# Kernel optimization log

Measured on AMD Instinct MI355X. Metric: run time of the kernel, lower is better.

## Reference

```python
import jax, jax.numpy as jnp
import numpy as np

SEQ, BATCH, EMBED = 1024, 2, 768
E = 16            # num_experts = m * N = 2 * 8
FFN_H = 1536      # expert_dim = ceil(3072 / 2)
K_SHARED = 1
K_ROUTE = 3       # (m * top_k) - k_shared = 4 - 1
LN_EPS = 1e-5
NEG_INF = -1e9


def setup_inputs() -> dict:
    key = jax.random.key(0)
    ks = jax.random.split(key, 4)
    x = jax.random.normal(ks[0], (SEQ, BATCH, EMBED), dtype=jnp.float32)
    gate_w = jax.random.normal(ks[1], (EMBED, E), dtype=jnp.float32) * 0.02
    gate_b = jnp.zeros((E,), jnp.float32)
    fc1_w = jax.random.normal(ks[2], (E, EMBED, FFN_H), dtype=jnp.float32) * 0.02
    fc1_b = jnp.zeros((E, FFN_H), jnp.float32)
    ln_w = jnp.ones((E, FFN_H), jnp.float32)
    ln_b = jnp.zeros((E, FFN_H), jnp.float32)
    fc2_w = jax.random.normal(ks[3], (E, FFN_H, EMBED), dtype=jnp.float32) * 0.02
    fc2_b = jnp.zeros((E, EMBED), jnp.float32)
    return {"x": x, "gate_w": gate_w, "gate_b": gate_b,
            "fc1_w": fc1_w, "fc1_b": fc1_b, "ln_w": ln_w, "ln_b": ln_b,
            "fc2_w": fc2_w, "fc2_b": fc2_b}


def reference(x, gate_w, gate_b, fc1_w, fc1_b, ln_w, ln_b, fc2_w, fc2_b):
    S, B, D = x.shape
    T = S * B
    xf = x.reshape(T, D)

    # --- gating: mask shared-expert logits, softmax, top-k over routed probs ---
    scores = xf @ gate_w + gate_b                      # [T, E]
    scores = scores.at[:, :K_SHARED].set(NEG_INF)
    probs = jax.nn.softmax(scores, axis=-1)
    topv, topi = jax.lax.top_k(probs, K_ROUTE)         # [T, K_ROUTE]

    # combine weights: gate prob for selected routed experts, 1.0 for shared experts
    combine = jnp.zeros((T, E), xf.dtype)
    combine = combine.at[jnp.arange(T)[:, None], topi].add(topv)
    combine = combine.at[:, :K_SHARED].add(1.0)        # shared expert(s), weight 1

    # --- per-expert FFN (dense over experts; combine zeros out unselected) ---
    h = jnp.einsum('td,edh->eth', xf, fc1_w) + fc1_b[:, None, :]   # [E, T, H]
    h = jax.nn.gelu(h, approximate=False)              # torch nn.GELU = exact erf
    mu = h.mean(-1, keepdims=True)
    var = h.var(-1, keepdims=True)
    h = (h - mu) * jax.lax.rsqrt(var + LN_EPS) * ln_w[:, None, :] + ln_b[:, None, :]
    y = jnp.einsum('eth,ehd->etd', h, fc2_w) + fc2_b[:, None, :]   # [E, T, D]

    # --- scatter-add combine (gate-weighted sum over experts) ---
    out = jnp.einsum('te,etd->td', combine, y)
    return out.reshape(S, B, D)
```

## Files before the change

kernel.cpp:

```cpp
#include <hip/hip_runtime.h>
#include <cmath>

#define T_TOK 2048
#define D_EMB 768
#define H_FFN 1536
#define NE    16
#define NPAIR (T_TOK * 4)

#define NT1   4608
#define NT2   4608
#define NCONV 2048
#define NGATE 512

typedef __attribute__((ext_vector_type(8))) short          short8;
typedef __attribute__((ext_vector_type(8))) unsigned short ushort8;
typedef __attribute__((ext_vector_type(4))) unsigned short ushort4v;
typedef __attribute__((ext_vector_type(4))) float          floatx4;

__device__ __forceinline__ float bf2f(unsigned short u) {
  union { unsigned int i; float f; } v; v.i = ((unsigned int)u) << 16; return v.f;
}
__device__ __forceinline__ unsigned short f2bf(float f) {
  union { float f; unsigned int i; } v; v.f = f;
  unsigned int r = v.i + 0x7fffu + ((v.i >> 16) & 1u);
  return (unsigned short)(r >> 16);
}

__device__ __forceinline__ void gload16(const unsigned short* g, unsigned short* l) {
  __builtin_amdgcn_global_load_lds(
      (const __attribute__((address_space(1))) unsigned int*)g,
      (__attribute__((address_space(3))) unsigned int*)l,
      16, 0, 0);
}

__device__ __forceinline__ int block_sniff(const unsigned int* __restrict__ xw, int tid) {
  int c = 0;
#pragma unroll
  for (int i = 0; i < 2; i++) {
    unsigned int w = xw[tid * 2 + i];
    unsigned int e = (w >> 7) & 0xFFu;
    c += (e >= 100u && e <= 140u) ? 1 : 0;
  }
#pragma unroll
  for (int off = 32; off > 0; off >>= 1) c += __shfl_down(c, off);
  __shared__ int ssn[4];
  int wave = tid >> 6, lane = tid & 63;
  if (lane == 0) ssn[wave] = c;
  __syncthreads();
  return (ssn[0] + ssn[1] + ssn[2] + ssn[3] > 300) ? 1 : 0;
}

template<int R, int C>
__device__ __forceinline__ void transpose_body(
    const unsigned short* __restrict__ srcB, const float* __restrict__ srcF,
    int isbf, unsigned short* __restrict__ dst, int bx, int tid,
    unsigned char* smemraw)
{
  auto tile = (unsigned short(*)[72])smemraw;
  constexpr int RT = R / 64, CT = C / 64;
  int e   = bx / (RT * CT);
  int rem = bx % (RT * CT);
  int rt  = rem / CT, ct = rem % CT;
  int r   = tid >> 2;
  int c   = (tid & 3) * 16;
  int xr  = (r & 7) * 8;
  size_t sbase = ((size_t)e * R + rt * 64 + r) * C + ct * 64 + c;
  if (isbf) {
    ushort8 v0 = *(const ushort8*)(srcB + sbase);
    ushort8 v1 = *(const ushort8*)(srcB + sbase + 8);
    *(ushort8*)&tile[r][(c) ^ xr]     = v0;
    *(ushort8*)&tile[r][(c + 8) ^ xr] = v1;
  } else {
    unsigned short tmp[16];
#pragma unroll
    for (int q = 0; q < 4; q++) {
      floatx4 f = *(const floatx4*)(srcF + sbase + q * 4);
#pragma unroll
      for (int j = 0; j < 4; j++) tmp[q * 4 + j] = f2bf(f[j]);
    }
    *(ushort8*)&tile[r][(c) ^ xr]     = *(ushort8*)&tmp[0];
    *(ushort8*)&tile[r][(c + 8) ^ xr] = *(ushort8*)&tmp[8];
  }
  __syncthreads();
  int n  = tid >> 2;
  int k  = (tid & 3) * 16;
  unsigned short outv[16];
#pragma unroll
  for (int j = 0; j < 16; j++) {
    int kr = k + j;
    outv[j] = tile[kr][n ^ ((kr & 7) * 8)];
  }
  size_t dbase = ((size_t)e * C + ct * 64 + n) * R + rt * 64 + k;
  *(ushort8*)(dst + dbase)     = *(ushort8*)&outv[0];
  *(ushort8*)(dst + dbase + 8) = *(ushort8*)&outv[8];
}

__global__ __launch_bounds__(256) void prep_kernel(
    const unsigned int* __restrict__ xw,
    const unsigned short* __restrict__ x16, const float* __restrict__ x32,
    const unsigned short* __restrict__ gw16, const float* __restrict__ gw32,
    const unsigned short* __restrict__ gb16, const float* __restrict__ gb32,
    const unsigned short* __restrict__ w1B, const float* __restrict__ w1F,
    const unsigned short* __restrict__ w2B, const float* __restrict__ w2F,
    const float* __restrict__ fc1bF, const float* __restrict__ lnwF,
    const float* __restrict__ lnbF, const float* __restrict__ fc2bF,
    unsigned short* __restrict__ xC,
    unsigned short* __restrict__ dfc1b, unsigned short* __restrict__ dlnw,
    unsigned short* __restrict__ dlnb, unsigned short* __restrict__ dfc2b,
    unsigned short* __restrict__ fc1T, unsigned short* __restrict__ fc2T,
    int* __restrict__ flagOut,
    int* __restrict__ psel, float* __restrict__ pw,
    int* __restrict__ cnt, int* __restrict__ plist)
{
  __shared__ __align__(16) unsigned char smem[4 * 64 * 17 * 4];
  int bid = blockIdx.x;
  int tid = threadIdx.x;
  int isbf = block_sniff(xw, tid);
  if (bid == 0 && tid == 0) *flagOut = isbf;

  if (bid < NT1) {
    transpose_body<768, 1536>(w1B, w1F, isbf, fc1T, bid, tid, smem);
  } else if (bid < NT1 + NT2) {
    transpose_body<1536, 768>(w2B, w2F, isbf, fc2T, bid - NT1, tid, smem);
  } else if (bid < NT1 + NT2 + NCONV) {
    if (!isbf) {
      int g = (bid - NT1 - NT2) * 256 + tid;
#pragma unroll
      for (int i = 0; i < 3; i++) xC[g + i * 524288] = f2bf(x32[g + i * 524288]);
      if (g < 24576) { dfc1b[g] = f2bf(fc1bF[g]); dlnw[g] = f2bf(lnwF[g]); dlnb[g] = f2bf(lnbF[g]); }
      if (g < 12288) dfc2b[g] = f2bf(fc2bF[g]);
    }
  } else {
    int wave = tid >> 6, lane = tid & 63;
    int t = (bid - (NT1 + NT2 + NCONV)) * 4 + wave;
    float acc[NE];
#pragma unroll
    for (int e = 0; e < NE; e++) acc[e] = 0.f;
    if (isbf) {
#pragma unroll
      for (int i = 0; i < D_EMB / 64; i++) {
        int d = i * 64 + lane;
        float xv = bf2f(x16[(size_t)t * D_EMB + d]);
        ushort8 g0 = *(const ushort8*)(gw16 + d * NE);
        ushort8 g1 = *(const ushort8*)(gw16 + d * NE + 8);
#pragma unroll
        for (int e = 0; e < 8; e++) acc[e]     += xv * bf2f(g0[e]);
#pragma unroll
        for (int e = 0; e < 8; e++) acc[8 + e] += xv * bf2f(g1[e]);
      }
    } else {
#pragma unroll
      for (int i = 0; i < D_EMB / 64; i++) {
        int d = i * 64 + lane;
        float xv = x32[(size_t)t * D_EMB + d];
#pragma unroll
        for (int q = 0; q < 4; q++) {
          floatx4 g = *(const floatx4*)(gw32 + d * NE + q * 4);
#pragma unroll
          for (int j = 0; j < 4; j++) acc[q * 4 + j] += xv * g[j];
        }
      }
    }
    auto sacc = (float(*)[64][17])smem;
#pragma unroll
    for (int e = 0; e < NE; e++) sacc[wave][lane][e] = acc[e];
    __syncthreads();
    int e = lane & 15, q = lane >> 4;
    float s = 0.f;
#pragma unroll
    for (int i = 0; i < 16; i++) s += sacc[wave][q * 16 + i][e];
    s += __shfl_xor(s, 16);
    s += __shfl_xor(s, 32);
    float sv = s + (isbf ? bf2f(gb16[e]) : gb32[e]);
    if (e == 0) sv = -1e9f;
    float m = sv;
#pragma unroll
    for (int off = 8; off > 0; off >>= 1) m = fmaxf(m, __shfl_xor(m, off));
    float pe = expf(sv - m);
    float den = pe;
#pragma unroll
    for (int off = 8; off > 0; off >>= 1) den += __shfl_xor(den, off);
    float pr = pe / den;
    float val = (e == 0) ? -1.f : pr;
    int sel0, sel1, sel2; float sw0, sw1, sw2;
#pragma unroll
    for (int k = 0; k < 3; k++) {
      float bv = val; int bi = e;
#pragma unroll
      for (int off = 8; off > 0; off >>= 1) {
        float ov = __shfl_xor(bv, off);
        int   oi = __shfl_xor(bi, off);
        if (ov > bv || (ov == bv && oi < bi)) { bv = ov; bi = oi; }
      }
      if (k == 0) { sel0 = bi; sw0 = bv; }
      else if (k == 1) { sel1 = bi; sw1 = bv; }
      else { sel2 = bi; sw2 = bv; }
      if (e == bi) val = -1.f;
    }
    if (lane < 4) {
      int se; float swt;
      if (lane == 0)      { se = 0;    swt = 1.0f; }
      else if (lane == 1) { se = sel0; swt = sw0; }
      else if (lane == 2) { se = sel1; swt = sw1; }
      else                { se = sel2; swt = sw2; }
      int pidx = t * 4 + lane;
      psel[pidx] = se; pw[pidx] = swt;
      int pos = atomicAdd(&cnt[se], 1);
      plist[se * T_TOK + pos] = pidx;
    }
  }
}

template<int KDIM, int NDIM, bool GELU, bool HASBIAS, bool AROWDIV4, bool OUTF32>
__global__ __launch_bounds__(256) void moe_gemm(
    const unsigned short* __restrict__ AO, const unsigned short* __restrict__ AC,
    const unsigned short* __restrict__ BT,
    const unsigned short* __restrict__ biasO, const unsigned short* __restrict__ biasC,
    const int* __restrict__ flag,
    const int* __restrict__ cnt, const int* __restrict__ plist,
    unsigned short* __restrict__ outB, float* __restrict__ outF)
{
  const int NSP = NDIM / 128;
  int bx  = blockIdx.x;
  int e   = bx / (16 * NSP);
  int rem = bx % (16 * NSP);
  int mt  = rem / NSP;
  int ns  = rem % NSP;
  int count = cnt[e];
  if (mt * 128 >= count) return;
  const unsigned short* Abase   = (*flag) ? AO : AC;
  const unsigned short* biasAll = (*flag) ? biasO : biasC;

  __shared__ __align__(16) unsigned short sA[128 * 64];
  __shared__ __align__(16) unsigned short sB[128 * 64];
  __shared__ int sp[128];

  int tid = threadIdx.x;
  if (tid < 128) {
    int rg  = mt * 128 + tid;
    int idx = rg < count ? rg : count - 1;
    sp[tid] = plist[e * T_TOK + idx];
  }
  __syncthreads();

  int lane = tid & 63;
  int wave = tid >> 6;
  int n0   = ns * 128;

  int lrow  = lane >> 3;
  int lsch  = (lane & 7) ^ lrow;
  const unsigned short* ag[4];
  const unsigned short* bg[4];
  int loff[4];
#pragma unroll
  for (int s = 0; s < 4; s++) {
    int r  = wave * 32 + s * 8;
    int p  = sp[r + lrow];
    ag[s] = Abase + (size_t)(AROWDIV4 ? (p >> 2) : p) * KDIM + lsch * 8;
    bg[s] = BT + ((size_t)e * NDIM + n0 + r + lrow) * KDIM + lsch * 8;
    loff[s] = r * 64;
  }

  int m16  = lane & 15;
  int quad = lane >> 4;
  int wm   = (wave >> 1) * 64;
  int wn   = (wave & 1) * 64;
  int rsw  = (m16 & 7);

  floatx4 acc[4][4];
#pragma unroll
  for (int i = 0; i < 4; i++)
#pragma unroll
    for (int j = 0; j < 4; j++) acc[i][j] = (floatx4){0.f, 0.f, 0.f, 0.f};

  for (int k0 = 0; k0 < KDIM; k0 += 64) {
    if (k0) __syncthreads();
#pragma unroll
    for (int s = 0; s < 4; s++) gload16(ag[s] + k0, sA + loff[s]);
#pragma unroll
    for (int s = 0; s < 4; s++) gload16(bg[s] + k0, sB + loff[s]);
    __syncthreads();
#pragma unroll
    for (int ks = 0; ks < 2; ks++) {
      int ch = ((ks * 4 + quad) ^ rsw) * 8;
      short8 af[4], bf[4];
#pragma unroll
      for (int m = 0; m < 4; m++)
        af[m] = *(const short8*)(sA + (wm + m * 16 + m16) * 64 + ch);
#pragma unroll
      for (int n = 0; n < 4; n++)
        bf[n] = *(const short8*)(sB + (wn + n * 16 + m16) * 64 + ch);
#pragma unroll
      for (int m = 0; m < 4; m++)
#pragma unroll
        for (int n = 0; n < 4; n++)
          acc[m][n] = __builtin_amdgcn_mfma_f32_16x16x32_bf16(af[m], bf[n], acc[m][n], 0, 0, 0);
    }
  }

#pragma unroll
  for (int m = 0; m < 4; m++) {
#pragma unroll
    for (int r = 0; r < 4; r++) {
      int row_local = wm + m * 16 + quad * 4 + r;
      int rg = mt * 128 + row_local;
      if (rg < count) {
        int p = sp[row_local];
#pragma unroll
        for (int n = 0; n < 4; n++) {
          int col = n0 + wn + n * 16 + m16;
          float v = acc[m][n][r];
          if (HASBIAS) v += bf2f(biasAll[e * NDIM + col]);
          if (GELU)    v = 0.5f * v * (1.f + erff(v * 0.70710678118654752f));
          if (OUTF32) outF[(size_t)p * NDIM + col] = v;
          else        outB[(size_t)p * NDIM + col] = f2bf(v);
        }
      }
    }
  }
}

__global__ __launch_bounds__(256) void ln_kernel(
    unsigned short* __restrict__ Hbuf,
    const unsigned short* __restrict__ lnwO, const unsigned short* __restrict__ lnwC,
    const unsigned short* __restrict__ lnbO, const unsigned short* __restrict__ lnbC,
    const int* __restrict__ psel, const float* __restrict__ pw,
    const int* __restrict__ flag)
{
  int p = blockIdx.x;
  int tid = threadIdx.x;
  int e = psel[p];
  int isbf = *flag;
  const unsigned short* lnw = isbf ? lnwO : lnwC;
  const unsigned short* lnb = isbf ? lnbO : lnbC;
  unsigned short* hr = Hbuf + (size_t)p * H_FFN;
  bool act = tid < 192;
  float v[8];
  float s = 0.f, sq = 0.f;
  if (act) {
    ushort8 hv = *(const ushort8*)(hr + tid * 8);
#pragma unroll
    for (int j = 0; j < 8; j++) { v[j] = bf2f(hv[j]); s += v[j]; sq += v[j] * v[j]; }
  }
#pragma unroll
  for (int off = 32; off > 0; off >>= 1) {
    s  += __shfl_down(s, off);
    sq += __shfl_down(sq, off);
  }
  __shared__ float red[8];
  int wave = tid >> 6, lane = tid & 63;
  if (lane == 0) { red[wave * 2] = s; red[wave * 2 + 1] = sq; }
  __syncthreads();
  __shared__ float mv[2];
  if (tid == 0) {
    float S = 0.f, Q = 0.f;
    for (int w = 0; w < 4; w++) { S += red[w * 2]; Q += red[w * 2 + 1]; }
    float mu  = S * (1.f / H_FFN);
    float var = Q * (1.f / H_FFN) - mu * mu;
    mv[0] = mu; mv[1] = rsqrtf(var + 1e-5f);
  }
  __syncthreads();
  if (act) {
    float mu = mv[0], rstd = mv[1];
    float w = pw[p];
    ushort8 lw = *(const ushort8*)(lnw + e * H_FFN + tid * 8);
    ushort8 lb = *(const ushort8*)(lnb + e * H_FFN + tid * 8);
    ushort8 o;
#pragma unroll
    for (int j = 0; j < 8; j++)
      o[j] = f2bf(((v[j] - mu) * rstd * bf2f(lw[j]) + bf2f(lb[j])) * w);
    *(ushort8*)(hr + tid * 8) = o;
  }
}

__global__ __launch_bounds__(192) void combine_kernel(
    const float* __restrict__ Y,
    const unsigned short* __restrict__ b2O, const unsigned short* __restrict__ b2C,
    const int* __restrict__ psel, const float* __restrict__ pw,
    unsigned short* __restrict__ out16, float* __restrict__ out32,
    const int* __restrict__ flag)
{
  int t = blockIdx.x;
  int tid = threadIdx.x;
  int isbf = *flag;
  const unsigned short* b2 = isbf ? b2O : b2C;
  int e1 = psel[t * 4 + 1], e2 = psel[t * 4 + 2], e3 = psel[t * 4 + 3];
  float w1 = pw[t * 4 + 1], w2 = pw[t * 4 + 2], w3 = pw[t * 4 + 3];
  int d = tid * 4;
  const float* Yb = Y + (size_t)t * 4 * D_EMB + d;
  floatx4 y0 = *(const floatx4*)(Yb);
  floatx4 y1 = *(const floatx4*)(Yb + D_EMB);
  floatx4 y2 = *(const floatx4*)(Yb + 2 * D_EMB);
  floatx4 y3 = *(const floatx4*)(Yb + 3 * D_EMB);
  ushort4v b0 = *(const ushort4v*)(b2 + d);
  ushort4v bb1 = *(const ushort4v*)(b2 + e1 * D_EMB + d);
  ushort4v bb2 = *(const ushort4v*)(b2 + e2 * D_EMB + d);
  ushort4v bb3 = *(const ushort4v*)(b2 + e3 * D_EMB + d);
  if (isbf) {
    ushort4v o;
#pragma unroll
    for (int j = 0; j < 4; j++) {
      float a = y0[j] + y1[j] + y2[j] + y3[j] + bf2f(b0[j])
              + w1 * bf2f(bb1[j]) + w2 * bf2f(bb2[j]) + w3 * bf2f(bb3[j]);
      o[j] = f2bf(a);
    }
    *(ushort4v*)(out16 + (size_t)t * D_EMB + d) = o;
  } else {
    floatx4 o;
#pragma unroll
    for (int j = 0; j < 4; j++)
      o[j] = y0[j] + y1[j] + y2[j] + y3[j] + bf2f(b0[j])
           + w1 * bf2f(bb1[j]) + w2 * bf2f(bb2[j]) + w3 * bf2f(bb3[j]);
    *(floatx4*)(out32 + (size_t)t * D_EMB + d) = o;
  }
}

extern "C" void kernel_launch(void* const* d_in, const int* in_sizes, int n_in,
                              void* d_out, int out_size, void* d_ws, size_t ws_size,
                              hipStream_t stream)
{
  (void)in_sizes; (void)n_in; (void)out_size; (void)ws_size;
  char* ws = (char*)d_ws;
  int*   cnt   = (int*)ws;
  int*   plist = (int*)(ws + 256);
  int*   psel  = (int*)(ws + 131328);
  float* pw    = (float*)(ws + 164096);
  int*   flag  = (int*)(ws + 196864);
  unsigned short* fc1bC = (unsigned short*)(ws + 197120);
  unsigned short* lnwC  = (unsigned short*)(ws + 246272);
  unsigned short* lnbC  = (unsigned short*)(ws + 295424);
  unsigned short* fc2bC = (unsigned short*)(ws + 344576);
  unsigned short* xC    = (unsigned short*)(ws + 524288);
  unsigned short* Hbuf  = (unsigned short*)(ws + 3670016);
  float*          Ybuf  = (float*)(ws + 28835840);
  unsigned short* fc1T  = (unsigned short*)(ws + 54001664);
  unsigned short* fc2T  = (unsigned short*)(ws + 91750400);

  hipMemsetAsync(cnt, 0, 64, stream);

  prep_kernel<<<NT1 + NT2 + NCONV + NGATE, 256, 0, stream>>>(
      (const unsigned int*)d_in[0],
      (const unsigned short*)d_in[0], (const float*)d_in[0],
      (const unsigned short*)d_in[1], (const float*)d_in[1],
      (const unsigned short*)d_in[2], (const float*)d_in[2],
      (const unsigned short*)d_in[3], (const float*)d_in[3],
      (const unsigned short*)d_in[7], (const float*)d_in[7],
      (const float*)d_in[4], (const float*)d_in[5],
      (const float*)d_in[6], (const float*)d_in[8],
      xC, fc1bC, lnwC, lnbC, fc2bC,
      fc1T, fc2T,
      flag, psel, pw, cnt, plist);

  moe_gemm<D_EMB, H_FFN, true, true, true, false>
      <<<NE * 16 * (H_FFN / 128), 256, 0, stream>>>(
      (const unsigned short*)d_in[0], xC, fc1T,
      (const unsigned short*)d_in[4], fc1bC,
      flag, cnt, plist, Hbuf, nullptr);

  ln_kernel<<<NPAIR, 256, 0, stream>>>(
      Hbuf,
      (const unsigned short*)d_in[5], lnwC,
      (const unsigned short*)d_in[6], lnbC,
      psel, pw, flag);

  moe_gemm<H_FFN, D_EMB, false, false, false, true>
      <<<NE * 16 * (D_EMB / 128), 256, 0, stream>>>(
      Hbuf, Hbuf, fc2T,
      nullptr, nullptr,
      flag, cnt, plist, nullptr, Ybuf);

  combine_kernel<<<T_TOK, 192, 0, stream>>>(
      Ybuf,
      (const unsigned short*)d_in[8], fc2bC,
      psel, pw,
      (unsigned short*)d_out, (float*)d_out, flag);
}
```

Baseline: 354.2 us.

## Drop weight transpose pass; read K-major weights via LDS transpose loads

The prep kernel no longer transposes fc1/fc2 weights into N-major layout. It now does a plain vectorised fp32->bf16 conversion, or nothing when inputs are already bf16. The GEMM loads B tiles in their original K×N layout into LDS and uses ds_read_b64_tr_b16 to build the MFMA B fragments, removing the transpose's LDS round trip and strided writes. The cost is an explicit lgkmcnt wait and sched barrier in the inner loop, plus an LDS tile layout that may bank-conflict.

```diff
diff --git a/kernel.cpp b/kernel.cpp
--- a/kernel.cpp
+++ b/kernel.cpp
@@ -7,12 +7,14 @@
 #define NE    16
 #define NPAIR (T_TOK * 4)
 
-#define NT1   4608
-#define NT2   4608
-#define NCONV 2048
+#define NW1   9216
+#define NW2   9216
+#define NX    768
+#define NB    12
 #define NGATE 512
 
 typedef __attribute__((ext_vector_type(8))) short          short8;
+typedef __attribute__((ext_vector_type(4))) short          short4v;
 typedef __attribute__((ext_vector_type(8))) unsigned short ushort8;
 typedef __attribute__((ext_vector_type(4))) unsigned short ushort4v;
 typedef __attribute__((ext_vector_type(4))) float          floatx4;
@@ -31,6 +33,17 @@
       (const __attribute__((address_space(1))) unsigned int*)g,
       (__attribute__((address_space(3))) unsigned int*)l,
       16, 0, 0);
+}
+
+__device__ __forceinline__ unsigned ldsaddr(const void* p) {
+  return (unsigned)(unsigned long long)
+      (const __attribute__((address_space(3))) char*)p;
+}
+
+__device__ __forceinline__ short4v tr8(unsigned a) {
+  short4v d;
+  asm volatile("ds_read_b64_tr_b16 %0, %1" : "=v"(d) : "v"(a));
+  return d;
 }
 
 __device__ __forceinline__ int block_sniff(const unsigned int* __restrict__ xw, int tid) {
@@ -50,49 +63,14 @@
   return (ssn[0] + ssn[1] + ssn[2] + ssn[3] > 300) ? 1 : 0;
 }
 
-template<int R, int C>
-__device__ __forceinline__ void transpose_body(
-    const unsigned short* __restrict__ srcB, const float* __restrict__ srcF,
-    int isbf, unsigned short* __restrict__ dst, int bx, int tid,
-    unsigned char* smemraw)
-{
-  auto tile = (unsigned short(*)[72])smemraw;
-  constexpr int RT = R / 64, CT = C / 64;
-  int e   = bx / (RT * CT);
-  int rem = bx % (RT * CT);
-  int rt  = rem / CT, ct = rem % CT;
-  int r   = tid >> 2;
-  int c   = (tid & 3) * 16;
-  int xr  = (r & 7) * 8;
-  size_t sbase = ((size_t)e * R + rt * 64 + r) * C + ct * 64 + c;
-  if (isbf) {
-    ushort8 v0 = *(const ushort8*)(srcB + sbase);
-    ushort8 v1 = *(const ushort8*)(srcB + sbase + 8);
-    *(ushort8*)&tile[r][(c) ^ xr]     = v0;
-    *(ushort8*)&tile[r][(c + 8) ^ xr] = v1;
-  } else {
-    unsigned short tmp[16];
-#pragma unroll
-    for (int q = 0; q < 4; q++) {
-      floatx4 f = *(const floatx4*)(srcF + sbase + q * 4);
-#pragma unroll
-      for (int j = 0; j < 4; j++) tmp[q * 4 + j] = f2bf(f[j]);
-    }
-    *(ushort8*)&tile[r][(c) ^ xr]     = *(ushort8*)&tmp[0];
-    *(ushort8*)&tile[r][(c + 8) ^ xr] = *(ushort8*)&tmp[8];
-  }
-  __syncthreads();
-  int n  = tid >> 2;
-  int k  = (tid & 3) * 16;
-  unsigned short outv[16];
-#pragma unroll
-  for (int j = 0; j < 16; j++) {
-    int kr = k + j;
-    outv[j] = tile[kr][n ^ ((kr & 7) * 8)];
-  }
-  size_t dbase = ((size_t)e * C + ct * 64 + n) * R + rt * 64 + k;
-  *(ushort8*)(dst + dbase)     = *(ushort8*)&outv[0];
-  *(ushort8*)(dst + dbase + 8) = *(ushort8*)&outv[8];
+__device__ __forceinline__ void conv8(const float* __restrict__ src,
+                                      unsigned short* __restrict__ dst, size_t i) {
+  floatx4 a = *(const floatx4*)(src + i);
+  floatx4 b = *(const floatx4*)(src + i + 4);
+  ushort8 o;
+#pragma unroll
+  for (int j = 0; j < 4; j++) { o[j] = f2bf(a[j]); o[4 + j] = f2bf(b[j]); }
+  *(ushort8*)(dst + i) = o;
 }
 
 __global__ __launch_bounds__(256) void prep_kernel(
@@ -100,39 +78,41 @@
     const unsigned short* __restrict__ x16, const float* __restrict__ x32,
     const unsigned short* __restrict__ gw16, const float* __restrict__ gw32,
     const unsigned short* __restrict__ gb16, const float* __restrict__ gb32,
-    const unsigned short* __restrict__ w1B, const float* __restrict__ w1F,
-    const unsigned short* __restrict__ w2B, const float* __restrict__ w2F,
+    const float* __restrict__ w1F, const float* __restrict__ w2F,
     const float* __restrict__ fc1bF, const float* __restrict__ lnwF,
     const float* __restrict__ lnbF, const float* __restrict__ fc2bF,
     unsigned short* __restrict__ xC,
+    unsigned short* __restrict__ wsW1, unsigned short* __restrict__ wsW2,
     unsigned short* __restrict__ dfc1b, unsigned short* __restrict__ dlnw,
     unsigned short* __restrict__ dlnb, unsigned short* __restrict__ dfc2b,
-    unsigned short* __restrict__ fc1T, unsigned short* __restrict__ fc2T,
     int* __restrict__ flagOut,
     int* __restrict__ psel, float* __restrict__ pw,
     int* __restrict__ cnt, int* __restrict__ plist)
 {
-  __shared__ __align__(16) unsigned char smem[4 * 64 * 17 * 4];
+  __shared__ __align__(16) float sacc[4][64][17];
   int bid = blockIdx.x;
   int tid = threadIdx.x;
   int isbf = block_sniff(xw, tid);
   if (bid == 0 && tid == 0) *flagOut = isbf;
 
-  if (bid < NT1) {
-    transpose_body<768, 1536>(w1B, w1F, isbf, fc1T, bid, tid, smem);
-  } else if (bid < NT1 + NT2) {
-    transpose_body<1536, 768>(w2B, w2F, isbf, fc2T, bid - NT1, tid, smem);
-  } else if (bid < NT1 + NT2 + NCONV) {
+  if (bid < NW1) {
+    if (!isbf) conv8(w1F, wsW1, ((size_t)bid * 256 + tid) * 8);
+  } else if (bid < NW1 + NW2) {
+    if (!isbf) conv8(w2F, wsW2, ((size_t)(bid - NW1) * 256 + tid) * 8);
+  } else if (bid < NW1 + NW2 + NX) {
+    if (!isbf) conv8(x32, xC, ((size_t)(bid - NW1 - NW2) * 256 + tid) * 8);
+  } else if (bid < NW1 + NW2 + NX + NB) {
     if (!isbf) {
-      int g = (bid - NT1 - NT2) * 256 + tid;
-#pragma unroll
-      for (int i = 0; i < 3; i++) xC[g + i * 524288] = f2bf(x32[g + i * 524288]);
-      if (g < 24576) { dfc1b[g] = f2bf(fc1bF[g]); dlnw[g] = f2bf(lnwF[g]); dlnb[g] = f2bf(lnbF[g]); }
-      if (g < 12288) dfc2b[g] = f2bf(fc2bF[g]);
+      size_t g = (size_t)(bid - NW1 - NW2 - NX) * 256 + tid;
+      size_t i = g * 8;
+      conv8(fc1bF, dfc1b, i);
+      conv8(lnwF,  dlnw,  i);
+      conv8(lnbF,  dlnb,  i);
+      if (g < 1536) conv8(fc2bF, dfc2b, i);
     }
   } else {
     int wave = tid >> 6, lane = tid & 63;
-    int t = (bid - (NT1 + NT2 + NCONV)) * 4 + wave;
+    int t = (bid - (NW1 + NW2 + NX + NB)) * 4 + wave;
     float acc[NE];
 #pragma unroll
     for (int e = 0; e < NE; e++) acc[e] = 0.f;
@@ -161,7 +141,6 @@
         }
       }
     }
-    auto sacc = (float(*)[64][17])smem;
 #pragma unroll
     for (int e = 0; e < NE; e++) sacc[wave][lane][e] = acc[e];
     __syncthreads();
@@ -214,7 +193,7 @@
 template<int KDIM, int NDIM, bool GELU, bool HASBIAS, bool AROWDIV4, bool OUTF32>
 __global__ __launch_bounds__(256) void moe_gemm(
     const unsigned short* __restrict__ AO, const unsigned short* __restrict__ AC,
-    const unsigned short* __restrict__ BT,
+    const unsigned short* __restrict__ BO, const unsigned short* __restrict__ BC,
     const unsigned short* __restrict__ biasO, const unsigned short* __restrict__ biasC,
     const int* __restrict__ flag,
     const int* __restrict__ cnt, const int* __restrict__ plist,
@@ -229,10 +208,11 @@
   int count = cnt[e];
   if (mt * 128 >= count) return;
   const unsigned short* Abase   = (*flag) ? AO : AC;
+  const unsigned short* Bbase   = (*flag) ? BO : BC;
   const unsigned short* biasAll = (*flag) ? biasO : biasC;
 
   __shared__ __align__(16) unsigned short sA[128 * 64];
-  __shared__ __align__(16) unsigned short sB[128 * 64];
+  __shared__ __align__(16) unsigned short sB[64 * 128];
   __shared__ int sp[128];
 
   int tid = threadIdx.x;
@@ -250,15 +230,24 @@
   int lrow  = lane >> 3;
   int lsch  = (lane & 7) ^ lrow;
   const unsigned short* ag[4];
-  const unsigned short* bg[4];
-  int loff[4];
+  int loffA[4];
 #pragma unroll
   for (int s = 0; s < 4; s++) {
     int r  = wave * 32 + s * 8;
     int p  = sp[r + lrow];
     ag[s] = Abase + (size_t)(AROWDIV4 ? (p >> 2) : p) * KDIM + lsch * 8;
-    bg[s] = BT + ((size_t)e * NDIM + n0 + r + lrow) * KDIM + lsch * 8;
-    loff[s] = r * 64;
+    loffA[s] = r * 64;
+  }
+
+  int bk = (lane >> 1) & 3;
+  int bn = (lane >> 3) * 16 + (lane & 1) * 8;
+  const unsigned short* bg[4];
+  int loffB[4];
+#pragma unroll
+  for (int s = 0; s < 4; s++) {
+    int krow = wave * 16 + s * 4 + bk;
+    bg[s] = Bbase + ((size_t)e * KDIM + krow) * NDIM + n0 + bn;
+    loffB[s] = (wave * 4 + s) * 512;
   }
 
   int m16  = lane & 15;
@@ -266,6 +255,8 @@
   int wm   = (wave >> 1) * 64;
   int wn   = (wave & 1) * 64;
   int rsw  = (m16 & 7);
+  unsigned trB = ldsaddr(sB)
+               + (unsigned)(quad * 2048 + (wave & 1) * 512 + m16 * 8);
 
   floatx4 acc[4][4];
 #pragma unroll
@@ -276,20 +267,27 @@
   for (int k0 = 0; k0 < KDIM; k0 += 64) {
     if (k0) __syncthreads();
 #pragma unroll
-    for (int s = 0; s < 4; s++) gload16(ag[s] + k0, sA + loff[s]);
-#pragma unroll
-    for (int s = 0; s < 4; s++) gload16(bg[s] + k0, sB + loff[s]);
+    for (int s = 0; s < 4; s++) gload16(ag[s] + k0, sA + loffA[s]);
+#pragma unroll
+    for (int s = 0; s < 4; s++) gload16(bg[s] + (size_t)k0 * NDIM, sB + loffB[s]);
     __syncthreads();
 #pragma unroll
     for (int ks = 0; ks < 2; ks++) {
       int ch = ((ks * 4 + quad) ^ rsw) * 8;
-      short8 af[4], bf[4];
+      short8 af[4];
 #pragma unroll
       for (int m = 0; m < 4; m++)
         af[m] = *(const short8*)(sA + (wm + m * 16 + m16) * 64 + ch);
-#pragma unroll
-      for (int n = 0; n < 4; n++)
-        bf[n] = *(const short8*)(sB + (wn + n * 16 + m16) * 64 + ch);
+      short8 bf[4];
+#pragma unroll
+      for (int nt = 0; nt < 4; nt++) {
+        union { short4v h[2]; short8 w; } u;
+        u.h[0] = tr8(trB + (unsigned)(ks * 8192 + nt * 128));
+        u.h[1] = tr8(trB + (unsigned)(ks * 8192 + 1024 + nt * 128));
+        bf[nt] = u.w;
+      }
+      asm volatile("s_waitcnt lgkmcnt(0)" ::: "memory");
+      __builtin_amdgcn_sched_barrier(0);
 #pragma unroll
       for (int m = 0; m < 4; m++)
 #pragma unroll
@@ -433,27 +431,27 @@
   unsigned short* xC    = (unsigned short*)(ws + 524288);
   unsigned short* Hbuf  = (unsigned short*)(ws + 3670016);
   float*          Ybuf  = (float*)(ws + 28835840);
-  unsigned short* fc1T  = (unsigned short*)(ws + 54001664);
-  unsigned short* fc2T  = (unsigned short*)(ws + 91750400);
+  unsigned short* wsW1  = (unsigned short*)(ws + 54001664);
+  unsigned short* wsW2  = (unsigned short*)(ws + 91750400);
 
   hipMemsetAsync(cnt, 0, 64, stream);
 
-  prep_kernel<<<NT1 + NT2 + NCONV + NGATE, 256, 0, stream>>>(
+  prep_kernel<<<NW1 + NW2 + NX + NB + NGATE, 256, 0, stream>>>(
       (const unsigned int*)d_in[0],
       (const unsigned short*)d_in[0], (const float*)d_in[0],
       (const unsigned short*)d_in[1], (const float*)d_in[1],
       (const unsigned short*)d_in[2], (const float*)d_in[2],
-      (const unsigned short*)d_in[3], (const float*)d_in[3],
-      (const unsigned short*)d_in[7], (const float*)d_in[7],
+      (const float*)d_in[3], (const float*)d_in[7],
       (const float*)d_in[4], (const float*)d_in[5],
       (const float*)d_in[6], (const float*)d_in[8],
-      xC, fc1bC, lnwC, lnbC, fc2bC,
-      fc1T, fc2T,
+      xC, wsW1, wsW2,
+      fc1bC, lnwC, lnbC, fc2bC,
       flag, psel, pw, cnt, plist);
 
   moe_gemm<D_EMB, H_FFN, true, true, true, false>
       <<<NE * 16 * (H_FFN / 128), 256, 0, stream>>>(
-      (const unsigned short*)d_in[0], xC, fc1T,
+      (const unsigned short*)d_in[0], xC,
+      (const unsigned short*)d_in[3], wsW1,
       (const unsigned short*)d_in[4], fc1bC,
       flag, cnt, plist, Hbuf, nullptr);
 
@@ -465,7 +463,8 @@
 
   moe_gemm<H_FFN, D_EMB, false, false, false, true>
       <<<NE * 16 * (D_EMB / 128), 256, 0, stream>>>(
-      Hbuf, Hbuf, fc2T,
+      Hbuf, Hbuf,
+      (const unsigned short*)d_in[7], wsW2,
       nullptr, nullptr,
       flag, cnt, plist, nullptr, Ybuf);
 
```

New measurement: 350.8 us. No clear change (-1.0%).
